# Performance work log

Hardware: AMD Instinct MI355X
Metric: run time of the kernel (lower is better)

The kernel has to match this reference:

```python
import jax, jax.numpy as jnp
import numpy as np

N_HEAD = 16

def rel_shift(x):
    # x: (qlen, klen, B, n). Pad one zero column at front of klen axis,
    # reinterpret as (klen+1, qlen, B, n), drop first row, reshape back.
    qlen, klen, b, n = x.shape
    x_pad = jnp.pad(x, ((0, 0), (1, 0), (0, 0), (0, 0)))
    x_pad = x_pad.reshape(klen + 1, qlen, b, n)
    return x_pad[1:].reshape(qlen, klen, b, n)

def setup_inputs() -> dict:
    key = jax.random.key(0)
    ks = jax.random.split(key, 9)
    qlen = klen = 1024
    B = 4
    d_model = 1024
    d_head = d_model // N_HEAD
    q = jax.random.normal(ks[0], (qlen, B, d_model), jnp.float32)
    K = jax.random.normal(ks[1], (klen, B, d_model), jnp.float32)
    V = jax.random.normal(ks[2], (klen, B, d_model), jnp.float32)
    mask = jax.random.bernoulli(ks[3], 0.1, (1, klen, B, 1))
    r = jax.random.normal(ks[4], (klen, d_model), jnp.float32)
    u = jax.random.normal(ks[5], (N_HEAD, d_head), jnp.float32) * 0.02
    v = jax.random.normal(ks[6], (N_HEAD, d_head), jnp.float32) * 0.02
    Wr = jax.random.normal(ks[7], (d_model, d_model), jnp.float32) / np.sqrt(d_model)
    br = jax.random.normal(ks[8], (d_model,), jnp.float32) * 0.02
    return {"q": q, "K": K, "V": V, "mask": mask, "r": r, "u": u, "v": v, "Wr": Wr, "br": br}

def reference(q, K, V, mask, r, u, v, Wr, br):
    qlen, bsz, d_model = q.shape
    klen = K.shape[0]
    d_head = d_model // N_HEAD
    qh = q.reshape(qlen, bsz, N_HEAD, d_head)
    Kh = K.reshape(klen, bsz, N_HEAD, d_head)
    Vh = V.reshape(klen, bsz, N_HEAD, d_head)
    rh = (r @ Wr.T + br).reshape(klen, N_HEAD, d_head)  # r_net projection
    AC = jnp.einsum('ibnd,jbnd->ijbn', qh + u, Kh)
    BD = rel_shift(jnp.einsum('ibnd,jnd->ijbn', qh + v, rh))
    score = (AC + BD) / jnp.sqrt(jnp.asarray(d_head, q.dtype))
    # mask (1,klen,B,1) broadcasts over qlen and heads (torch repeats over heads)
    score = jnp.where(mask, jnp.asarray(-1e9, score.dtype), score)
    weight = jax.nn.softmax(score, axis=1)
    out = jnp.einsum('ijbn,jbnd->ibnd', weight, Vh).reshape(qlen, bsz, d_model)
    return out, weight.mean(axis=-1)
```

## Files before the change

### kernel.cpp

```cpp
#include <hip/hip_runtime.h>
#include <hip/hip_fp16.h>
#include <stdint.h>


#define L 1024
#define BATCH 4
#define NH 16
#define DH 64
#define DM 1024
#define TI 16
#define NJT 16
#define BD_ST 1028
#define BDP_ST 1032
#define WT_ST 40
#define SCALE 0.125f
#define CS 0.18033688011112042f

typedef __attribute__((ext_vector_type(8))) short short8;
typedef __attribute__((ext_vector_type(4))) float f32x4;

static __device__ __forceinline__ unsigned short f2bf(float f) {
    union { float f; unsigned int u; } x; x.f = f;
    return (unsigned short)((x.u + 0x7fffu + ((x.u >> 16) & 1u)) >> 16);
}
static __device__ __forceinline__ float bf2f(unsigned short h) {
    union { unsigned int u; float f; } x; x.u = ((unsigned int)h) << 16;
    return x.f;
}
static __device__ __forceinline__ unsigned short f2h(float f) {
    __half h = __float2half(f);
    union { __half h; unsigned short s; } x; x.h = h; return x.s;
}
static __device__ __forceinline__ float h2f(unsigned short s) {
    union { __half h; unsigned short s; } x; x.s = s; return __half2float(x.h);
}
static __device__ __forceinline__ unsigned short* usp(void* base, int byteoff) {
    return (unsigned short*)((char*)base + byteoff);
}
static __device__ __forceinline__ short8 ld8(const void* base, int byteoff) {
    return *(const short8*)((const char*)base + byteoff);
}
static __device__ __forceinline__ float fexp2(float x) {
#if __has_builtin(__builtin_amdgcn_exp2f)
    return __builtin_amdgcn_exp2f(x);
#else
    return __expf(x * 0.6931471805599453f);
#endif
}
#define SW128(row, colByte) ((((row) * 128) + (colByte)) ^ (((row) & 7) << 4))

__global__ __launch_bounds__(256) void rh_gemm_mfma(
    const float* __restrict__ r, const float* __restrict__ Wr,
    const float* __restrict__ br, unsigned short* __restrict__ rhb)
{
    __shared__ unsigned short rT[64 * 64];
    __shared__ unsigned short wT[64 * 64];
    const int c0 = blockIdx.x * 64, m0 = blockIdx.y * 64;
    const int tid = threadIdx.x;
    const int w = tid >> 6, lane = tid & 63, lr = lane & 15, lg = lane >> 4;
    f32x4 acc[4] = {};

    for (int kt = 0; kt < 16; ++kt) {
        const int k0 = kt * 64;
        __syncthreads();
        const int row = tid >> 2, cb = (tid & 3) * 16;
#pragma unroll
        for (int q4 = 0; q4 < 4; ++q4) {
            float4 rv = *(const float4*)(r + (size_t)(c0 + row) * DM + k0 + cb + q4 * 4);
            unsigned short* p = usp(rT, SW128(row, (cb + q4 * 4) * 2));
            p[0] = f2bf(rv.x); p[1] = f2bf(rv.y); p[2] = f2bf(rv.z); p[3] = f2bf(rv.w);
            float4 wv = *(const float4*)(Wr + (size_t)(m0 + row) * DM + k0 + cb + q4 * 4);
            unsigned short* pw = usp(wT, SW128(row, (cb + q4 * 4) * 2));
            pw[0] = f2bf(wv.x); pw[1] = f2bf(wv.y); pw[2] = f2bf(wv.z); pw[3] = f2bf(wv.w);
        }
        __syncthreads();
#pragma unroll
        for (int mch = 0; mch < 4; ++mch)
#pragma unroll
            for (int kh = 0; kh < 2; ++kh) {
                short8 a  = ld8(rT, SW128(w * 16 + lr,   (kh * 32 + lg * 8) * 2));
                short8 bb = ld8(wT, SW128(mch * 16 + lr, (kh * 32 + lg * 8) * 2));
                acc[mch] = __builtin_amdgcn_mfma_f32_16x16x32_bf16(a, bb, acc[mch], 0, 0, 0);
            }
    }
#pragma unroll
    for (int mch = 0; mch < 4; ++mch)
#pragma unroll
        for (int r2 = 0; r2 < 4; ++r2) {
            const int c = c0 + w * 16 + lg * 4 + r2;
            const int d = mch * 16 + lr;
            const float val = acc[mch][r2] + br[m0 + d];
            rhb[((size_t)blockIdx.y * L + c) * DH + d] = f2bf(val);
        }
}

__global__ __launch_bounds__(256) void rh_gemm_kernel(
    const float* __restrict__ r, const float* __restrict__ Wr,
    const float* __restrict__ br, float* __restrict__ rhf)
{
    __shared__ float As[16][65];
    __shared__ float Bs[16][65];
    const int j0 = blockIdx.x * 64;
    const int m0 = blockIdx.y * 64;
    const int tid = threadIdx.x;
    const int ty = tid >> 4, tx = tid & 15;
    float acc[4][4] = {};

    for (int k0 = 0; k0 < DM; k0 += 16) {
        const int row = tid >> 2, c4 = (tid & 3) << 2;
        float4 av = *(const float4*)(r  + (size_t)(j0 + row) * DM + k0 + c4);
        float4 bv = *(const float4*)(Wr + (size_t)(m0 + row) * DM + k0 + c4);
        __syncthreads();
        As[c4 + 0][row] = av.x; As[c4 + 1][row] = av.y;
        As[c4 + 2][row] = av.z; As[c4 + 3][row] = av.w;
        Bs[c4 + 0][row] = bv.x; Bs[c4 + 1][row] = bv.y;
        Bs[c4 + 2][row] = bv.z; Bs[c4 + 3][row] = bv.w;
        __syncthreads();
#pragma unroll
        for (int k = 0; k < 16; ++k) {
            float a[4], bb[4];
#pragma unroll
            for (int t = 0; t < 4; ++t) { a[t] = As[k][ty * 4 + t]; bb[t] = Bs[k][tx * 4 + t]; }
#pragma unroll
            for (int ii = 0; ii < 4; ++ii)
#pragma unroll
                for (int jj = 0; jj < 4; ++jj)
                    acc[ii][jj] = fmaf(a[ii], bb[jj], acc[ii][jj]);
        }
    }
#pragma unroll
    for (int ii = 0; ii < 4; ++ii) {
        const int row = j0 + ty * 4 + ii;
#pragma unroll
        for (int jj = 0; jj < 4; ++jj) {
            const int col = m0 + tx * 4 + jj;
            rhf[(size_t)row * DM + col] = acc[ii][jj] + br[col];
        }
    }
}

__global__ __launch_bounds__(256) void prepass_kernel(
    const float* __restrict__ Kg, const float* __restrict__ Vg,
    unsigned short* __restrict__ Kbf, unsigned short* __restrict__ Vtb)
{
    __shared__ unsigned short tile[64][80];
    const int j0 = blockIdx.x * 64;
    const int b = blockIdx.y, n = blockIdx.z;
    const int bn = b * NH + n;
    const int tid = threadIdx.x;

    for (int idx = tid; idx < 64 * 16; idx += 256) {
        const int jr = idx >> 4, s4 = (idx & 15) * 4;
        const size_t src = ((size_t)(j0 + jr) * BATCH + b) * DM + n * DH + s4;
        float4 kv = *(const float4*)(Kg + src);
        ushort4 o;
        o.x = f2bf(kv.x); o.y = f2bf(kv.y); o.z = f2bf(kv.z); o.w = f2bf(kv.w);
        *(ushort4*)(Kbf + ((size_t)bn * L + j0 + jr) * DH + s4) = o;
        float4 vv4 = *(const float4*)(Vg + src);
        tile[s4 + 0][jr] = f2bf(vv4.x); tile[s4 + 1][jr] = f2bf(vv4.y);
        tile[s4 + 2][jr] = f2bf(vv4.z); tile[s4 + 3][jr] = f2bf(vv4.w);
    }
    __syncthreads();
    for (int idx = tid; idx < 64 * 8; idx += 256) {
        const int d = idx >> 3, p8 = (idx & 7) * 8;
        short8 o = *(const short8*)&tile[d][p8];
        *(short8*)(Vtb + ((size_t)bn * DH + d) * L + j0 + p8) = o;
    }
}

__global__ __launch_bounds__(256) void wm_reduce_kernel(
    const unsigned short* __restrict__ Wf, const float* __restrict__ rdeng,
    float* __restrict__ wm_out)
{
    const int ib = blockIdx.x;
    const int gq = blockIdx.y;
    const int b  = blockIdx.z;
    const int tid = threadIdx.x;
    const int w = tid >> 6, lane = tid & 63, lr = lane & 15, lg = lane >> 4;
    const int i = ib * 16 + lr;

    float rd[NH];
#pragma unroll
    for (int n = 0; n < NH; ++n)
        rd[n] = rdeng[((size_t)(b * NH + n) << 10) + i];

#pragma unroll
    for (int k = 0; k < 4; ++k) {
        const int gc = gq * 16 + w * 4 + k;
        float a0 = 0.f, a1 = 0.f, a2 = 0.f, a3 = 0.f;
#pragma unroll
        for (int n = 0; n < NH; ++n) {
            const int bn = b * NH + n;
            ushort4 wv = *(const ushort4*)(Wf +
                (((size_t)(bn * 64 + ib) * 64 + gc) * 64 + lane) * 4);
            a0 += bf2f(wv.x) * rd[n]; a1 += bf2f(wv.y) * rd[n];
            a2 += bf2f(wv.z) * rd[n]; a3 += bf2f(wv.w) * rd[n];
        }
        const size_t o = ((size_t)i * L + gc * 16 + lg * 4) * BATCH + b;
        wm_out[o]             = a0;
        wm_out[o + BATCH]     = a1;
        wm_out[o + 2 * BATCH] = a2;
        wm_out[o + 3 * BATCH] = a3;
    }
}

#define CHUNK_BODY(CHUNK, JC, KF0, KF1)                                       \
    {                                                                         \
        const int chunk_ = (CHUNK);                                           \
        const int jc_ = (JC);                                                 \
        short8 nk0_, nk1_;                                                    \
        const bool pf_ = (chunk_ + 2) < 16;                                   \
        if (pf_) {                                                            \
            const int jn_ = jwbase + (chunk_ + 2) * 16 + lr;                  \
            nk0_ = *(const short8*)(Kpane + (size_t)jn_ * DH + lg * 8);       \
            nk1_ = *(const short8*)(Kpane + (size_t)jn_ * DH + 32 + lg * 8);  \
        }                                                                     \
        f32x4 acc_ = {0.f, 0.f, 0.f, 0.f};                                    \
        acc_ = __builtin_amdgcn_mfma_f32_16x16x32_bf16(KF0, qu_a[0], acc_, 0, 0, 0); \
        acc_ = __builtin_amdgcn_mfma_f32_16x16x32_bf16(KF1, qu_a[1], acc_, 0, 0, 0); \
        const int jq_ = jc_ + lg * 4;                                         \
        const unsigned int m4_ = *(const unsigned int*)&mblk[jq_];            \
        const ushort4 bdq_ = *(const ushort4*)&BD[lr * BD_ST + jq_];          \
        ushort4 wpack_;                                                       \
        _Pragma("unroll")                                                     \
        for (int r2 = 0; r2 < 4; ++r2) {                                      \
            const unsigned short bdh_ =                                       \
                (r2 == 0) ? bdq_.x : (r2 == 1) ? bdq_.y : (r2 == 2) ? bdq_.z : bdq_.w; \
            const float mo_ = ((m4_ >> (8 * r2)) & 0xffu) ? -1e9f : 0.f;      \
            const float s_ = fminf(acc_[r2] + h2f(bdh_) + mo_, 126.f);        \
            const float wg_ = fexp2(s_);                                      \
            dl += wg_;                                                        \
            ((unsigned short*)&wpack_)[r2] = f2bf(wg_);                       \
        }                                                                     \
        *(ushort4*)(WtW + lr * WT_ST + ((jc_ >> 4) & 1) * 16 + lg * 4) = wpack_; \
        {          \
            union { ushort4 u4; unsigned long long u64; } cw_;                \
            cw_.u4 = wpack_;                                                  \
            __builtin_nontemporal_store(cw_.u64,                              \
                (unsigned long long*)(W_ws + wsbase + (((size_t)(jc_ >> 4)) * 64 + lane) * 4)); \
        }                                                                     \
        if (pf_) { KF0 = nk0_; KF1 = nk1_; }                                  \
    }

#define BD_BODY(CT, RB0, RB1)                                                 \
    {                                                                         \
        const int ct_ = (CT);                                                 \
        const int c0_ = ct_ * 64;                                             \
        short8 nr0_, nr1_;                                                    \
        const bool pf_ = (ct_ + 2) < 16;                                      \
        if (pf_) {                                                            \
            nr0_ = *(const short8*)(rpane + (size_t)((ct_ + 2) * 64 + ccol) * DH + lg * 8); \
            nr1_ = *(const short8*)(rpane + (size_t)((ct_ + 2) * 64 + ccol) * DH + 32 + lg * 8); \
        }                                                                     \
        f32x4 acc_ = {0.f, 0.f, 0.f, 0.f};                                    \
        acc_ = __builtin_amdgcn_mfma_f32_16x16x32_bf16(qv_a[0], RB0, acc_, 0, 0, 0); \
        acc_ = __builtin_amdgcn_mfma_f32_16x16x32_bf16(qv_a[1], RB1, acc_, 0, 0, 0); \
        const int c_ = c0_ + ccol;                                            \
        _Pragma("unroll")                                                     \
        for (int r2 = 0; r2 < 4; ++r2) {                                      \
            const int ilp_ = lg * 4 + r2;                                     \
            const unsigned short hv_ = f2h(acc_[r2]);                         \
            const int j1_ = c_ + i0 + ilp_ - 1023;                            \
            if (j1_ >= 0) BD[ilp_ * BD_ST + j1_] = hv_;                       \
            const int j2_ = c_ + i0 + ilp_ + 1;                               \
            if (ilp_ >= 1 && j2_ <= 1023) BD[(ilp_ - 1) * BD_ST + j2_] = hv_; \
        }                                                                     \
        {                           \
            short8 ra0_ = *(const short8*)(rpane + (size_t)(c0_ + col16) * DH + kq); \
            short8 ra1_ = *(const short8*)(rpane + (size_t)(c0_ + col16) * DH + kq + 8); \
            float s16_ = 0.f;                                                 \
            _Pragma("unroll")                                                 \
            for (int e = 0; e < 8; ++e) {                                     \
                s16_ = fmaf(qv16[e],     bf2f((unsigned short)ra0_[e]), s16_);\
                s16_ = fmaf(qv16[e + 8], bf2f((unsigned short)ra1_[e]), s16_);\
            }                                                                 \
            s16_ += __shfl_xor(s16_, 1);                                      \
            s16_ += __shfl_xor(s16_, 2);                                      \
            const int j16_ = c0_ + col16 + i0 + 17;                           \
            if ((tid & 3) == 0 && j16_ <= 1023)                               \
                BD[15 * BD_ST + j16_] = f2h(s16_);                            \
        }                                                                     \
        if (pf_) { RB0 = nr0_; RB1 = nr1_; }                                  \
    }

__global__ __launch_bounds__(256, 4) void attn_fused(
    const float* __restrict__ q,
    const unsigned short* __restrict__ Kbf, const unsigned short* __restrict__ Vtb,
    const unsigned char* __restrict__ maskp,
    const float* __restrict__ uu, const float* __restrict__ vvp,
    const unsigned short* __restrict__ rhb,
    float* __restrict__ out, unsigned short* __restrict__ W_ws,
    float* __restrict__ rdeng)
{
    __shared__ __align__(16) unsigned short BD[16 * BD_ST];
    __shared__ __align__(16) unsigned short Wt[4][16 * WT_ST];
    __shared__ unsigned char mblk[L];
    __shared__ float denomP[4][16];
    __shared__ float rdenom[16];
    __shared__ int mflags;

    const int lin = blockIdx.x;
    const int xcd = lin & 7, idx = lin >> 3;
    const int ib  = idx & 63;
    const int pane = xcd * 8 + (idx >> 6);
    const int b = pane >> 4, n = pane & 15;
    const int i0 = ib * 16;
    const int bn = pane;

    const int tid = threadIdx.x;
    const int w = tid >> 6, lane = tid & 63, lr = lane & 15, lg = lane >> 4;

    if (tid == 0) mflags = 0;
    __syncthreads();
    {
        int local = 0;
#pragma unroll 1
        for (int ww = tid; ww < 1024; ww += 256) {
            const unsigned int word = ((const unsigned int*)maskp)[ww];
            if (word == 0x3f800000u) local |= 1;
            else if (word & 0xffffff00u) local |= 2;
        }
        if (local) atomicOr(&mflags, local);
    }
    __syncthreads();
    {
        const int mtype = (mflags & 1) ? 2 : ((mflags & 2) ? 1 : 0);
#pragma unroll 1
        for (int j = tid; j < L; j += 256) {
            bool mv;
            if (mtype == 2)      mv = ((const float*)maskp)[j * BATCH + b] != 0.f;
            else if (mtype == 1) mv = maskp[j * BATCH + b] != 0;
            else                 mv = ((const int*)maskp)[j * BATCH + b] != 0;
            mblk[j] = mv ? 1 : 0;
        }
    }
    if (tid < 16) {
        const int jz = i0 + tid + 1;
        if (jz <= 1023) BD[tid * BD_ST + jz] = 0;
    }

    const float* qrow = q + ((size_t)(i0 + lr) * BATCH + b) * DM + n * DH;
    const float* urow = uu + n * DH;
    const float* vrow = vvp + n * DH;
    short8 qu_a[2], qv_a[2];
#pragma unroll
    for (int kh = 0; kh < 2; ++kh) {
        const int kb = kh * 32 + lg * 8;
        float4 qa = *(const float4*)(qrow + kb), qb = *(const float4*)(qrow + kb + 4);
        float4 ua = *(const float4*)(urow + kb), ub = *(const float4*)(urow + kb + 4);
        float4 va = *(const float4*)(vrow + kb), vb = *(const float4*)(vrow + kb + 4);
        short8 su, sv;
        su[0] = (short)f2bf((qa.x + ua.x) * CS); su[1] = (short)f2bf((qa.y + ua.y) * CS);
        su[2] = (short)f2bf((qa.z + ua.z) * CS); su[3] = (short)f2bf((qa.w + ua.w) * CS);
        su[4] = (short)f2bf((qb.x + ub.x) * CS); su[5] = (short)f2bf((qb.y + ub.y) * CS);
        su[6] = (short)f2bf((qb.z + ub.z) * CS); su[7] = (short)f2bf((qb.w + ub.w) * CS);
        sv[0] = (short)f2bf((qa.x + va.x) * CS); sv[1] = (short)f2bf((qa.y + va.y) * CS);
        sv[2] = (short)f2bf((qa.z + va.z) * CS); sv[3] = (short)f2bf((qa.w + va.w) * CS);
        sv[4] = (short)f2bf((qb.x + vb.x) * CS); sv[5] = (short)f2bf((qb.y + vb.y) * CS);
        sv[6] = (short)f2bf((qb.z + vb.z) * CS); sv[7] = (short)f2bf((qb.w + vb.w) * CS);
        qu_a[kh] = su; qv_a[kh] = sv;
    }
    float qv16[16];
    {
        const int kq0 = (tid & 3) * 16;
        if (i0 + 16 < L) {
            const float* q16 = q + ((size_t)(i0 + 16) * BATCH + b) * DM + n * DH;
#pragma unroll
            for (int e4 = 0; e4 < 4; ++e4) {
                float4 qa = *(const float4*)(q16 + kq0 + e4 * 4);
                float4 va = *(const float4*)(vrow + kq0 + e4 * 4);
                qv16[e4 * 4 + 0] = (qa.x + va.x) * CS; qv16[e4 * 4 + 1] = (qa.y + va.y) * CS;
                qv16[e4 * 4 + 2] = (qa.z + va.z) * CS; qv16[e4 * 4 + 3] = (qa.w + va.w) * CS;
            }
        } else {
#pragma unroll
            for (int e = 0; e < 16; ++e) qv16[e] = 0.f;
        }
    }

    {
        const unsigned short* rpane = rhb + (size_t)n * L * DH;
        const int ccol = w * 16 + lr;
        const int col16 = tid >> 2;
        const int kq = (tid & 3) * 16;
        short8 rbA0, rbA1, rbB0, rbB1;
        rbA0 = *(const short8*)(rpane + (size_t)ccol * DH + lg * 8);
        rbA1 = *(const short8*)(rpane + (size_t)ccol * DH + 32 + lg * 8);
        rbB0 = *(const short8*)(rpane + (size_t)(64 + ccol) * DH + lg * 8);
        rbB1 = *(const short8*)(rpane + (size_t)(64 + ccol) * DH + 32 + lg * 8);
#pragma unroll 1
        for (int ct2 = 0; ct2 < 8; ++ct2) {
            BD_BODY(ct2 * 2,     rbA0, rbA1);
            BD_BODY(ct2 * 2 + 1, rbB0, rbB1);
        }
    }
    __syncthreads();

    const unsigned short* Kpane = Kbf + (size_t)bn * L * DH;
    const unsigned short* Vpane = Vtb + (size_t)bn * DH * L;
    const int jwbase = w * 256;
    unsigned short* WtW = &Wt[w][0];
    f32x4 pv[4] = {};
    float dl = 0.f;
    const size_t wsbase = (((size_t)bn * 64 + ib) * 64) * 64 * 4;

    short8 kfA0, kfA1, kfB0, kfB1;
    kfA0 = *(const short8*)(Kpane + (size_t)(jwbase + lr) * DH + lg * 8);
    kfA1 = *(const short8*)(Kpane + (size_t)(jwbase + lr) * DH + 32 + lg * 8);
    kfB0 = *(const short8*)(Kpane + (size_t)(jwbase + 16 + lr) * DH + lg * 8);
    kfB1 = *(const short8*)(Kpane + (size_t)(jwbase + 16 + lr) * DH + 32 + lg * 8);

#pragma unroll 1
    for (int wi = 0; wi < 8; ++wi) {
        const int jbase32 = jwbase + wi * 32;
        short8 vf0, vf1, vf2, vf3;
        vf0 = *(const short8*)(Vpane + (size_t)(0 * 16 + lr) * L + jbase32 + lg * 8);
        vf1 = *(const short8*)(Vpane + (size_t)(1 * 16 + lr) * L + jbase32 + lg * 8);
        vf2 = *(const short8*)(Vpane + (size_t)(2 * 16 + lr) * L + jbase32 + lg * 8);
        vf3 = *(const short8*)(Vpane + (size_t)(3 * 16 + lr) * L + jbase32 + lg * 8);
        CHUNK_BODY(wi * 2,     jbase32,      kfA0, kfA1);
        CHUNK_BODY(wi * 2 + 1, jbase32 + 16, kfB0, kfB1);
        short8 afrag = *(const short8*)(WtW + lr * WT_ST + lg * 8);
        pv[0] = __builtin_amdgcn_mfma_f32_16x16x32_bf16(afrag, vf0, pv[0], 0, 0, 0);
        pv[1] = __builtin_amdgcn_mfma_f32_16x16x32_bf16(afrag, vf1, pv[1], 0, 0, 0);
        pv[2] = __builtin_amdgcn_mfma_f32_16x16x32_bf16(afrag, vf2, pv[2], 0, 0, 0);
        pv[3] = __builtin_amdgcn_mfma_f32_16x16x32_bf16(afrag, vf3, pv[3], 0, 0, 0);
    }

    dl += __shfl_xor(dl, 16, 64);
    dl += __shfl_xor(dl, 32, 64);
    if (lane < 16) denomP[w][lane] = dl;
    __syncthreads();

    {
        float* pvw = (float*)BD + w * 1024;
#pragma unroll
        for (int dch = 0; dch < 4; ++dch)
#pragma unroll
            for (int r2 = 0; r2 < 4; ++r2)
                pvw[(lg * 4 + r2) * 64 + dch * 16 + lr] = pv[dch][r2];
    }
    if (tid < 16) {
        const float dn = denomP[0][tid] + denomP[1][tid] + denomP[2][tid] + denomP[3][tid];
        rdenom[tid] = 1.f / dn;
        rdeng[((size_t)bn << 10) + i0 + tid] = 1.f / (dn * 16.f);
    }
    __syncthreads();

    {
        const float* pvwAll = (const float*)BD;
        const int il = tid >> 4, d0 = (tid & 15) * 4;
        float4 o  = *(const float4*)(pvwAll + 0 * 1024 + il * 64 + d0);
        float4 o1 = *(const float4*)(pvwAll + 1 * 1024 + il * 64 + d0);
        float4 o2 = *(const float4*)(pvwAll + 2 * 1024 + il * 64 + d0);
        float4 o3 = *(const float4*)(pvwAll + 3 * 1024 + il * 64 + d0);
        const float rs = rdenom[il];
        o.x = (o.x + o1.x + o2.x + o3.x) * rs;
        o.y = (o.y + o1.y + o2.y + o3.y) * rs;
        o.z = (o.z + o1.z + o2.z + o3.z) * rs;
        o.w = (o.w + o1.w + o2.w + o3.w) * rs;
        *(float4*)(out + ((size_t)(i0 + il) * BATCH + b) * DM + n * DH + d0) = o;
    }
}

template<int MODE>
__global__ __launch_bounds__(256, 2) void attn_legacy(
    const float* __restrict__ q,
    const void* __restrict__ Kp, const void* __restrict__ Vp,
    const unsigned char* __restrict__ maskp,
    const float* __restrict__ uu, const float* __restrict__ vvp,
    const void* __restrict__ rhp,
    float* __restrict__ out, float* __restrict__ wm_out)
{
    __shared__ unsigned short QU[16 * 64];
    __shared__ unsigned short QV[17 * 64];
    __shared__ unsigned short KR[(MODE == 1) ? 64 * 64 : 8];
    __shared__ unsigned short VT[(MODE == 1) ? 64 * 64 : 8];
    __shared__ unsigned short BDp[17 * BDP_ST];
    __shared__ unsigned short Wt[2][16 * 64];
    __shared__ unsigned char mblk[L];
    __shared__ float denomP[4][16];
    __shared__ float rdenom[16];
    __shared__ int mflags;

    const int i0 = blockIdx.x * TI;
    const int b  = blockIdx.y;
    const int n  = blockIdx.z;
    const int bn = b * NH + n;
    const int tid = threadIdx.x;
    const int w = tid >> 6, lane = tid & 63, lr = lane & 15, lg = lane >> 4;

    const unsigned short* Kbf = (const unsigned short*)Kp;
    const unsigned short* Vtb = (const unsigned short*)Vp;
    const unsigned short* rhb = (const unsigned short*)rhp;
    const float* Kg  = (const float*)Kp;
    const float* Vg  = (const float*)Vp;
    const float* rhf = (const float*)rhp;

    if (tid == 0) mflags = 0;
    __syncthreads();
    {
        int local = 0;
        for (int ww = tid; ww < 1024; ww += 256) {
            const unsigned int word = ((const unsigned int*)maskp)[ww];
            if (word == 0x3f800000u) local |= 1;
            else if (word & 0xffffff00u) local |= 2;
        }
        if (local) atomicOr(&mflags, local);
    }
    __syncthreads();
    {
        const int mtype = (mflags & 1) ? 2 : ((mflags & 2) ? 1 : 0);
        for (int j = tid; j < L; j += 256) {
            bool mv;
            if (mtype == 2)      mv = ((const float*)maskp)[j * BATCH + b] != 0.f;
            else if (mtype == 1) mv = maskp[j * BATCH + b] != 0;
            else                 mv = ((const int*)maskp)[j * BATCH + b] != 0;
            mblk[j] = mv ? 1 : 0;
        }
    }
    for (int idx = tid; idx < 17 * 64; idx += 256) {
        const int row = idx >> 6, d = idx & 63;
        const int gi = i0 + row;
        const float qval = (gi < L) ? q[((size_t)gi * BATCH + b) * DM + n * DH + d] : 0.f;
        *usp(QV, SW128(row, d * 2)) = f2bf((qval + vvp[n * DH + d]) * SCALE);
        if (row < 16) *usp(QU, SW128(row, d * 2)) = f2bf((qval + uu[n * DH + d]) * SCALE);
    }
    __syncthreads();

    for (int ct = 0; ct < 16; ++ct) {
        const int c0 = ct * 64;
        const int ccol = w * 16 + lr;
        if constexpr (MODE == 1) {
            __syncthreads();
            for (int idx = tid; idx < 64 * 16; idx += 256) {
                const int cr = idx >> 4, d4 = (idx & 15) * 4;
                float4 rv = *(const float4*)(rhf + (size_t)(c0 + cr) * DM + n * DH + d4);
                unsigned short* p = usp(KR, SW128(cr, d4 * 2));
                p[0] = f2bf(rv.x); p[1] = f2bf(rv.y); p[2] = f2bf(rv.z); p[3] = f2bf(rv.w);
            }
            __syncthreads();
        }
        f32x4 acc = {0.f, 0.f, 0.f, 0.f};
#pragma unroll
        for (int kh = 0; kh < 2; ++kh) {
            short8 a = ld8(QV, SW128(lr, (kh * 32 + lg * 8) * 2));
            short8 bb;
            if constexpr (MODE == 0)
                bb = *(const short8*)(rhb + ((size_t)n * L + c0 + ccol) * DH + kh * 32 + lg * 8);
            else
                bb = ld8(KR, SW128(ccol, (kh * 32 + lg * 8) * 2));
            acc = __builtin_amdgcn_mfma_f32_16x16x32_bf16(a, bb, acc, 0, 0, 0);
        }
#pragma unroll
        for (int r2 = 0; r2 < 4; ++r2)
            BDp[(lg * 4 + r2) * BDP_ST + c0 + ccol] = f2h(acc[r2]);
        {
            const int col = tid >> 2, kq = (tid & 3) * 16;
            float s16 = 0.f;
#pragma unroll
            for (int kk = 0; kk < 16; kk += 8) {
                short8 qa = ld8(QV, SW128(16, (kq + kk) * 2));
                short8 ra;
                if constexpr (MODE == 0)
                    ra = *(const short8*)(rhb + ((size_t)n * L + c0 + col) * DH + kq + kk);
                else
                    ra = ld8(KR, SW128(col, (kq + kk) * 2));
#pragma unroll
                for (int e = 0; e < 8; ++e)
                    s16 = fmaf(bf2f((unsigned short)qa[e]), bf2f((unsigned short)ra[e]), s16);
            }
            s16 += __shfl_xor(s16, 1);
            s16 += __shfl_xor(s16, 2);
            if ((tid & 3) == 0) BDp[16 * BDP_ST + c0 + col] = f2h(s16);
        }
    }

    const int jloc = w * 16 + lr;
    __syncthreads();

    f32x4 pv = {0.f, 0.f, 0.f, 0.f};
    float dl[4] = {0.f, 0.f, 0.f, 0.f};
    float tmp[4][NJT];
#pragma unroll
    for (int jt = 0; jt < NJT; ++jt) {
        const int j0 = jt * 64;
        const int gj = j0 + jloc;
        const int cur = jt & 1;
        if constexpr (MODE == 1) {
            __syncthreads();
            for (int idx = tid; idx < 64 * 16; idx += 256) {
                const int jr = idx >> 4, d4 = (idx & 15) * 4;
                const size_t src = ((size_t)(j0 + jr) * BATCH + b) * DM + n * DH + d4;
                float4 kv = *(const float4*)(Kg + src);
                unsigned short* p = usp(KR, SW128(jr, d4 * 2));
                p[0] = f2bf(kv.x); p[1] = f2bf(kv.y); p[2] = f2bf(kv.z); p[3] = f2bf(kv.w);
                float4 vv4 = *(const float4*)(Vg + src);
                *usp(VT, SW128(d4 + 0, jr * 2)) = f2bf(vv4.x);
                *usp(VT, SW128(d4 + 1, jr * 2)) = f2bf(vv4.y);
                *usp(VT, SW128(d4 + 2, jr * 2)) = f2bf(vv4.z);
                *usp(VT, SW128(d4 + 3, jr * 2)) = f2bf(vv4.w);
            }
            __syncthreads();
        }
        f32x4 acc = {0.f, 0.f, 0.f, 0.f};
#pragma unroll
        for (int kh = 0; kh < 2; ++kh) {
            short8 a = ld8(QU, SW128(lr, (kh * 32 + lg * 8) * 2));
            short8 bb;
            if constexpr (MODE == 0)
                bb = *(const short8*)(Kbf + ((size_t)bn * L + gj) * DH + kh * 32 + lg * 8);
            else
                bb = ld8(KR, SW128(jloc, (kh * 32 + lg * 8) * 2));
            acc = __builtin_amdgcn_mfma_f32_16x16x32_bf16(a, bb, acc, 0, 0, 0);
        }
        const bool msk = mblk[gj] != 0;
#pragma unroll
        for (int r2 = 0; r2 < 4; ++r2) {
            const int il = lg * 4 + r2;
            const int gi = i0 + il;
            const int t = gj - gi;
            float bd = 0.f;
            if (t != 1) {
                const int c = (t <= 0) ? (L - 1 + t) : (t - 2);
                bd = h2f(BDp[(il + (t >= 1 ? 1 : 0)) * BDP_ST + c]);
            }
            float s = acc[r2] + bd;
            if (msk) s = -1e9f;
            const float wgt = __expf(fminf(s, 80.f));
            dl[r2] += wgt;
            tmp[r2][jt] = wgt;
            *usp(Wt[cur], SW128(il, jloc * 2)) = f2bf(wgt);
        }
        __syncthreads();
#pragma unroll
        for (int kh = 0; kh < 2; ++kh) {
            short8 a = ld8(Wt[cur], SW128(lr, (kh * 32 + lg * 8) * 2));
            short8 bb;
            if constexpr (MODE == 0)
                bb = *(const short8*)(Vtb + ((size_t)bn * DH + jloc) * L + j0 + kh * 32 + lg * 8);
            else
                bb = ld8(VT, SW128(jloc, (kh * 32 + lg * 8) * 2));
            pv = __builtin_amdgcn_mfma_f32_16x16x32_bf16(a, bb, pv, 0, 0, 0);
        }
    }

#pragma unroll
    for (int r2 = 0; r2 < 4; ++r2) {
        float d = dl[r2];
        d += __shfl_xor(d, 1); d += __shfl_xor(d, 2);
        d += __shfl_xor(d, 4); d += __shfl_xor(d, 8);
        if (lr == 0) denomP[w][lg * 4 + r2] = d;
    }
    __syncthreads();
    if (tid < 16)
        rdenom[tid] = 1.f / (denomP[0][tid] + denomP[1][tid] + denomP[2][tid] + denomP[3][tid]);
    __syncthreads();

#pragma unroll
    for (int r2 = 0; r2 < 4; ++r2) {
        const int il = lg * 4 + r2;
        out[((size_t)(i0 + il) * BATCH + b) * DM + n * DH + w * 16 + lr] = pv[r2] * rdenom[il];
    }
#pragma unroll
    for (int r2 = 0; r2 < 4; ++r2) {
        const int il = lg * 4 + r2;
        const float rs = rdenom[il] * (1.f / 16.f);
#pragma unroll
        for (int jt = 0; jt < NJT; ++jt)
            atomicAdd(wm_out + ((size_t)(i0 + il) * L + jt * 64 + jloc) * BATCH + b,
                      tmp[r2][jt] * rs);
    }
}

extern "C" void kernel_launch(void* const* d_in, const int* in_sizes, int n_in,
                              void* d_out, int out_size, void* d_ws, size_t ws_size,
                              hipStream_t stream)
{
    (void)in_sizes; (void)n_in; (void)out_size;
    const float* q   = (const float*)d_in[0];
    const float* K   = (const float*)d_in[1];
    const float* V   = (const float*)d_in[2];
    const unsigned char* mask = (const unsigned char*)d_in[3];
    const float* r   = (const float*)d_in[4];
    const float* u   = (const float*)d_in[5];
    const float* v   = (const float*)d_in[6];
    const float* Wr  = (const float*)d_in[7];
    const float* br  = (const float*)d_in[8];

    float* out = (float*)d_out;
    float* wm  = out + (size_t)L * BATCH * DM;

    const size_t kvbytes = (size_t)BATCH * NH * L * DH * 2;
    const size_t rhbytes = (size_t)NH * L * DH * 2;
    const size_t wmbytes = (size_t)BATCH * NH * L * L * 2;
    const size_t rdbytes = (size_t)BATCH * NH * L * 4;

    if (ws_size >= 2 * kvbytes + rhbytes + wmbytes + rdbytes) {
        unsigned short* Kbf = (unsigned short*)d_ws;
        unsigned short* Vtb = Kbf + kvbytes / 2;
        unsigned short* rhb = Vtb + kvbytes / 2;
        unsigned short* Wws = rhb + rhbytes / 2;
        float* rdeng = (float*)(Wws + wmbytes / 2);
        rh_gemm_mfma<<<dim3(16, 16), 256, 0, stream>>>(r, Wr, br, rhb);
        prepass_kernel<<<dim3(16, 4, 16), 256, 0, stream>>>(K, V, Kbf, Vtb);
        attn_fused<<<dim3(4096), 256, 0, stream>>>(
            q, Kbf, Vtb, mask, u, v, rhb, out, Wws, rdeng);
        wm_reduce_kernel<<<dim3(64, 4, 4), 256, 0, stream>>>(Wws, rdeng, wm);
    } else if (ws_size >= 2 * kvbytes + rhbytes) {
        hipMemsetAsync(wm, 0, (size_t)L * L * BATCH * sizeof(float), stream);
        unsigned short* Kbf = (unsigned short*)d_ws;
        unsigned short* Vtb = Kbf + kvbytes / 2;
        unsigned short* rhb = Vtb + kvbytes / 2;
        rh_gemm_mfma<<<dim3(16, 16), 256, 0, stream>>>(r, Wr, br, rhb);
        prepass_kernel<<<dim3(16, 4, 16), 256, 0, stream>>>(K, V, Kbf, Vtb);
        attn_legacy<0><<<dim3(64, 4, 16), 256, 0, stream>>>(
            q, Kbf, Vtb, mask, u, v, rhb, out, wm);
    } else {
        hipMemsetAsync(wm, 0, (size_t)L * L * BATCH * sizeof(float), stream);
        float* rhf = (float*)d_ws;
        rh_gemm_kernel<<<dim3(16, 16), 256, 0, stream>>>(r, Wr, br, rhf);
        attn_legacy<1><<<dim3(64, 4, 16), 256, 0, stream>>>(
            q, K, V, mask, u, v, rhf, out, wm);
    }
}
```

Measured before the change: 293.7 us.

## Double attn_fused block to 512 threads and prebake mask into BD tile

Widens the fused attention block from 4 to 8 wavefronts, so each wave handles half as many key columns in both the BD projection and the softmax/PV loops, and the final cross-wave reduction sums 8 partials. The per-element mask select is removed from the hot loop: masked key columns are written as half-precision negative infinity into the BD shared tile before the score pass. The legacy fallback kernels and workspace-size checks are deleted, so the fused path always runs. The larger block raises per-block register and shared-memory demand and adds an extra barrier, and the fallback for small workspaces is gone.

```diff
diff --git a/kernel.cpp b/kernel.cpp
--- a/kernel.cpp
+++ b/kernel.cpp
@@ -15,6 +15,7 @@
 #define WT_ST 40
 #define SCALE 0.125f
 #define CS 0.18033688011112042f
+#define HNEGINF 0xFC00u
 
 typedef __attribute__((ext_vector_type(8))) short short8;
 typedef __attribute__((ext_vector_type(4))) float f32x4;
@@ -94,51 +95,6 @@
         }
 }
 
-__global__ __launch_bounds__(256) void rh_gemm_kernel(
-    const float* __restrict__ r, const float* __restrict__ Wr,
-    const float* __restrict__ br, float* __restrict__ rhf)
-{
-    __shared__ float As[16][65];
-    __shared__ float Bs[16][65];
-    const int j0 = blockIdx.x * 64;
-    const int m0 = blockIdx.y * 64;
-    const int tid = threadIdx.x;
-    const int ty = tid >> 4, tx = tid & 15;
-    float acc[4][4] = {};
-
-    for (int k0 = 0; k0 < DM; k0 += 16) {
-        const int row = tid >> 2, c4 = (tid & 3) << 2;
-        float4 av = *(const float4*)(r  + (size_t)(j0 + row) * DM + k0 + c4);
-        float4 bv = *(const float4*)(Wr + (size_t)(m0 + row) * DM + k0 + c4);
-        __syncthreads();
-        As[c4 + 0][row] = av.x; As[c4 + 1][row] = av.y;
-        As[c4 + 2][row] = av.z; As[c4 + 3][row] = av.w;
-        Bs[c4 + 0][row] = bv.x; Bs[c4 + 1][row] = bv.y;
-        Bs[c4 + 2][row] = bv.z; Bs[c4 + 3][row] = bv.w;
-        __syncthreads();
-#pragma unroll
-        for (int k = 0; k < 16; ++k) {
-            float a[4], bb[4];
-#pragma unroll
-            for (int t = 0; t < 4; ++t) { a[t] = As[k][ty * 4 + t]; bb[t] = Bs[k][tx * 4 + t]; }
-#pragma unroll
-            for (int ii = 0; ii < 4; ++ii)
-#pragma unroll
-                for (int jj = 0; jj < 4; ++jj)
-                    acc[ii][jj] = fmaf(a[ii], bb[jj], acc[ii][jj]);
-        }
-    }
-#pragma unroll
-    for (int ii = 0; ii < 4; ++ii) {
-        const int row = j0 + ty * 4 + ii;
-#pragma unroll
-        for (int jj = 0; jj < 4; ++jj) {
-            const int col = m0 + tx * 4 + jj;
-            rhf[(size_t)row * DM + col] = acc[ii][jj] + br[col];
-        }
-    }
-}
-
 __global__ __launch_bounds__(256) void prepass_kernel(
     const float* __restrict__ Kg, const float* __restrict__ Vg,
     unsigned short* __restrict__ Kbf, unsigned short* __restrict__ Vtb)
@@ -209,7 +165,7 @@
         const int chunk_ = (CHUNK);                                           \
         const int jc_ = (JC);                                                 \
         short8 nk0_, nk1_;                                                    \
-        const bool pf_ = (chunk_ + 2) < 16;                                   \
+        const bool pf_ = (chunk_ + 2) < 8;                                    \
         if (pf_) {                                                            \
             const int jn_ = jwbase + (chunk_ + 2) * 16 + lr;                  \
             nk0_ = *(const short8*)(Kpane + (size_t)jn_ * DH + lg * 8);       \
@@ -219,21 +175,19 @@
         acc_ = __builtin_amdgcn_mfma_f32_16x16x32_bf16(KF0, qu_a[0], acc_, 0, 0, 0); \
         acc_ = __builtin_amdgcn_mfma_f32_16x16x32_bf16(KF1, qu_a[1], acc_, 0, 0, 0); \
         const int jq_ = jc_ + lg * 4;                                         \
-        const unsigned int m4_ = *(const unsigned int*)&mblk[jq_];            \
         const ushort4 bdq_ = *(const ushort4*)&BD[lr * BD_ST + jq_];          \
         ushort4 wpack_;                                                       \
         _Pragma("unroll")                                                     \
         for (int r2 = 0; r2 < 4; ++r2) {                                      \
             const unsigned short bdh_ =                                       \
                 (r2 == 0) ? bdq_.x : (r2 == 1) ? bdq_.y : (r2 == 2) ? bdq_.z : bdq_.w; \
-            const float mo_ = ((m4_ >> (8 * r2)) & 0xffu) ? -1e9f : 0.f;      \
-            const float s_ = fminf(acc_[r2] + h2f(bdh_) + mo_, 126.f);        \
+            const float s_ = fminf(acc_[r2] + h2f(bdh_), 126.f);              \
             const float wg_ = fexp2(s_);                                      \
             dl += wg_;                                                        \
             ((unsigned short*)&wpack_)[r2] = f2bf(wg_);                       \
         }                                                                     \
         *(ushort4*)(WtW + lr * WT_ST + ((jc_ >> 4) & 1) * 16 + lg * 4) = wpack_; \
-        {          \
+        {                                         \
             union { ushort4 u4; unsigned long long u64; } cw_;                \
             cw_.u4 = wpack_;                                                  \
             __builtin_nontemporal_store(cw_.u64,                              \
@@ -245,12 +199,12 @@
 #define BD_BODY(CT, RB0, RB1)                                                 \
     {                                                                         \
         const int ct_ = (CT);                                                 \
-        const int c0_ = ct_ * 64;                                             \
+        const int c0_ = ct_ * 128;                                            \
         short8 nr0_, nr1_;                                                    \
-        const bool pf_ = (ct_ + 2) < 16;                                      \
+        const bool pf_ = (ct_ + 2) < 8;                                       \
         if (pf_) {                                                            \
-            nr0_ = *(const short8*)(rpane + (size_t)((ct_ + 2) * 64 + ccol) * DH + lg * 8); \
-            nr1_ = *(const short8*)(rpane + (size_t)((ct_ + 2) * 64 + ccol) * DH + 32 + lg * 8); \
+            nr0_ = *(const short8*)(rpane + (size_t)((ct_ + 2) * 128 + ccol) * DH + lg * 8); \
+            nr1_ = *(const short8*)(rpane + (size_t)((ct_ + 2) * 128 + ccol) * DH + 32 + lg * 8); \
         }                                                                     \
         f32x4 acc_ = {0.f, 0.f, 0.f, 0.f};                                    \
         acc_ = __builtin_amdgcn_mfma_f32_16x16x32_bf16(qv_a[0], RB0, acc_, 0, 0, 0); \
@@ -265,7 +219,7 @@
             const int j2_ = c_ + i0 + ilp_ + 1;                               \
             if (ilp_ >= 1 && j2_ <= 1023) BD[(ilp_ - 1) * BD_ST + j2_] = hv_; \
         }                                                                     \
-        {                           \
+        {         \
             short8 ra0_ = *(const short8*)(rpane + (size_t)(c0_ + col16) * DH + kq); \
             short8 ra1_ = *(const short8*)(rpane + (size_t)(c0_ + col16) * DH + kq + 8); \
             float s16_ = 0.f;                                                 \
@@ -283,7 +237,7 @@
         if (pf_) { RB0 = nr0_; RB1 = nr1_; }                                  \
     }
 
-__global__ __launch_bounds__(256, 4) void attn_fused(
+__global__ __launch_bounds__(512, 6) void attn_fused(
     const float* __restrict__ q,
     const unsigned short* __restrict__ Kbf, const unsigned short* __restrict__ Vtb,
     const unsigned char* __restrict__ maskp,
@@ -293,9 +247,9 @@
     float* __restrict__ rdeng)
 {
     __shared__ __align__(16) unsigned short BD[16 * BD_ST];
-    __shared__ __align__(16) unsigned short Wt[4][16 * WT_ST];
+    __shared__ __align__(16) unsigned short Wt[8][16 * WT_ST];
     __shared__ unsigned char mblk[L];
-    __shared__ float denomP[4][16];
+    __shared__ float denomP[8][16];
     __shared__ float rdenom[16];
     __shared__ int mflags;
 
@@ -315,7 +269,7 @@
     {
         int local = 0;
 #pragma unroll 1
-        for (int ww = tid; ww < 1024; ww += 256) {
+        for (int ww = tid; ww < 1024; ww += 512) {
             const unsigned int word = ((const unsigned int*)maskp)[ww];
             if (word == 0x3f800000u) local |= 1;
             else if (word & 0xffffff00u) local |= 2;
@@ -326,7 +280,7 @@
     {
         const int mtype = (mflags & 1) ? 2 : ((mflags & 2) ? 1 : 0);
 #pragma unroll 1
-        for (int j = tid; j < L; j += 256) {
+        for (int j = tid; j < L; j += 512) {
             bool mv;
             if (mtype == 2)      mv = ((const float*)maskp)[j * BATCH + b] != 0.f;
             else if (mtype == 1) mv = maskp[j * BATCH + b] != 0;
@@ -386,19 +340,29 @@
         short8 rbA0, rbA1, rbB0, rbB1;
         rbA0 = *(const short8*)(rpane + (size_t)ccol * DH + lg * 8);
         rbA1 = *(const short8*)(rpane + (size_t)ccol * DH + 32 + lg * 8);
-        rbB0 = *(const short8*)(rpane + (size_t)(64 + ccol) * DH + lg * 8);
-        rbB1 = *(const short8*)(rpane + (size_t)(64 + ccol) * DH + 32 + lg * 8);
+        rbB0 = *(const short8*)(rpane + (size_t)(128 + ccol) * DH + lg * 8);
+        rbB1 = *(const short8*)(rpane + (size_t)(128 + ccol) * DH + 32 + lg * 8);
 #pragma unroll 1
-        for (int ct2 = 0; ct2 < 8; ++ct2) {
+        for (int ct2 = 0; ct2 < 4; ++ct2) {
             BD_BODY(ct2 * 2,     rbA0, rbA1);
             BD_BODY(ct2 * 2 + 1, rbB0, rbB1);
         }
     }
     __syncthreads();
 
+#pragma unroll 1
+    for (int j = tid; j < L; j += 512) {
+        if (mblk[j]) {
+#pragma unroll
+            for (int il = 0; il < 16; ++il)
+                BD[il * BD_ST + j] = (unsigned short)HNEGINF;
+        }
+    }
+    __syncthreads();
+
     const unsigned short* Kpane = Kbf + (size_t)bn * L * DH;
     const unsigned short* Vpane = Vtb + (size_t)bn * DH * L;
-    const int jwbase = w * 256;
+    const int jwbase = w * 128;
     unsigned short* WtW = &Wt[w][0];
     f32x4 pv[4] = {};
     float dl = 0.f;
@@ -411,7 +375,7 @@
     kfB1 = *(const short8*)(Kpane + (size_t)(jwbase + 16 + lr) * DH + 32 + lg * 8);
 
 #pragma unroll 1
-    for (int wi = 0; wi < 8; ++wi) {
+    for (int wi = 0; wi < 4; ++wi) {
         const int jbase32 = jwbase + wi * 32;
         short8 vf0, vf1, vf2, vf3;
         vf0 = *(const short8*)(Vpane + (size_t)(0 * 16 + lr) * L + jbase32 + lg * 8);
@@ -441,235 +405,25 @@
                 pvw[(lg * 4 + r2) * 64 + dch * 16 + lr] = pv[dch][r2];
     }
     if (tid < 16) {
-        const float dn = denomP[0][tid] + denomP[1][tid] + denomP[2][tid] + denomP[3][tid];
+        const float dn = denomP[0][tid] + denomP[1][tid] + denomP[2][tid] + denomP[3][tid]
+                       + denomP[4][tid] + denomP[5][tid] + denomP[6][tid] + denomP[7][tid];
         rdenom[tid] = 1.f / dn;
         rdeng[((size_t)bn << 10) + i0 + tid] = 1.f / (dn * 16.f);
     }
     __syncthreads();
 
-    {
+    if (tid < 256) {
         const float* pvwAll = (const float*)BD;
         const int il = tid >> 4, d0 = (tid & 15) * 4;
-        float4 o  = *(const float4*)(pvwAll + 0 * 1024 + il * 64 + d0);
-        float4 o1 = *(const float4*)(pvwAll + 1 * 1024 + il * 64 + d0);
-        float4 o2 = *(const float4*)(pvwAll + 2 * 1024 + il * 64 + d0);
-        float4 o3 = *(const float4*)(pvwAll + 3 * 1024 + il * 64 + d0);
+        float4 o = *(const float4*)(pvwAll + il * 64 + d0);
+#pragma unroll
+        for (int ww = 1; ww < 8; ++ww) {
+            float4 ox = *(const float4*)(pvwAll + ww * 1024 + il * 64 + d0);
+            o.x += ox.x; o.y += ox.y; o.z += ox.z; o.w += ox.w;
+        }
         const float rs = rdenom[il];
-        o.x = (o.x + o1.x + o2.x + o3.x) * rs;
-        o.y = (o.y + o1.y + o2.y + o3.y) * rs;
-        o.z = (o.z + o1.z + o2.z + o3.z) * rs;
-        o.w = (o.w + o1.w + o2.w + o3.w) * rs;
+        o.x *= rs; o.y *= rs; o.z *= rs; o.w *= rs;
         *(float4*)(out + ((size_t)(i0 + il) * BATCH + b) * DM + n * DH + d0) = o;
-    }
-}
-
-template<int MODE>
-__global__ __launch_bounds__(256, 2) void attn_legacy(
-    const float* __restrict__ q,
-    const void* __restrict__ Kp, const void* __restrict__ Vp,
-    const unsigned char* __restrict__ maskp,
-    const float* __restrict__ uu, const float* __restrict__ vvp,
-    const void* __restrict__ rhp,
-    float* __restrict__ out, float* __restrict__ wm_out)
-{
-    __shared__ unsigned short QU[16 * 64];
-    __shared__ unsigned short QV[17 * 64];
-    __shared__ unsigned short KR[(MODE == 1) ? 64 * 64 : 8];
-    __shared__ unsigned short VT[(MODE == 1) ? 64 * 64 : 8];
-    __shared__ unsigned short BDp[17 * BDP_ST];
-    __shared__ unsigned short Wt[2][16 * 64];
-    __shared__ unsigned char mblk[L];
-    __shared__ float denomP[4][16];
-    __shared__ float rdenom[16];
-    __shared__ int mflags;
-
-    const int i0 = blockIdx.x * TI;
-    const int b  = blockIdx.y;
-    const int n  = blockIdx.z;
-    const int bn = b * NH + n;
-    const int tid = threadIdx.x;
-    const int w = tid >> 6, lane = tid & 63, lr = lane & 15, lg = lane >> 4;
-
-    const unsigned short* Kbf = (const unsigned short*)Kp;
-    const unsigned short* Vtb = (const unsigned short*)Vp;
-    const unsigned short* rhb = (const unsigned short*)rhp;
-    const float* Kg  = (const float*)Kp;
-    const float* Vg  = (const float*)Vp;
-    const float* rhf = (const float*)rhp;
-
-    if (tid == 0) mflags = 0;
-    __syncthreads();
-    {
-        int local = 0;
-        for (int ww = tid; ww < 1024; ww += 256) {
-            const unsigned int word = ((const unsigned int*)maskp)[ww];
-            if (word == 0x3f800000u) local |= 1;
-            else if (word & 0xffffff00u) local |= 2;
-        }
-        if (local) atomicOr(&mflags, local);
-    }
-    __syncthreads();
-    {
-        const int mtype = (mflags & 1) ? 2 : ((mflags & 2) ? 1 : 0);
-        for (int j = tid; j < L; j += 256) {
-            bool mv;
-            if (mtype == 2)      mv = ((const float*)maskp)[j * BATCH + b] != 0.f;
-            else if (mtype == 1) mv = maskp[j * BATCH + b] != 0;
-            else                 mv = ((const int*)maskp)[j * BATCH + b] != 0;
-            mblk[j] = mv ? 1 : 0;
-        }
-    }
-    for (int idx = tid; idx < 17 * 64; idx += 256) {
-        const int row = idx >> 6, d = idx & 63;
-        const int gi = i0 + row;
-        const float qval = (gi < L) ? q[((size_t)gi * BATCH + b) * DM + n * DH + d] : 0.f;
-        *usp(QV, SW128(row, d * 2)) = f2bf((qval + vvp[n * DH + d]) * SCALE);
-        if (row < 16) *usp(QU, SW128(row, d * 2)) = f2bf((qval + uu[n * DH + d]) * SCALE);
-    }
-    __syncthreads();
-
-    for (int ct = 0; ct < 16; ++ct) {
-        const int c0 = ct * 64;
-        const int ccol = w * 16 + lr;
-        if constexpr (MODE == 1) {
-            __syncthreads();
-            for (int idx = tid; idx < 64 * 16; idx += 256) {
-                const int cr = idx >> 4, d4 = (idx & 15) * 4;
-                float4 rv = *(const float4*)(rhf + (size_t)(c0 + cr) * DM + n * DH + d4);
-                unsigned short* p = usp(KR, SW128(cr, d4 * 2));
-                p[0] = f2bf(rv.x); p[1] = f2bf(rv.y); p[2] = f2bf(rv.z); p[3] = f2bf(rv.w);
-            }
-            __syncthreads();
-        }
-        f32x4 acc = {0.f, 0.f, 0.f, 0.f};
-#pragma unroll
-        for (int kh = 0; kh < 2; ++kh) {
-            short8 a = ld8(QV, SW128(lr, (kh * 32 + lg * 8) * 2));
-            short8 bb;
-            if constexpr (MODE == 0)
-                bb = *(const short8*)(rhb + ((size_t)n * L + c0 + ccol) * DH + kh * 32 + lg * 8);
-            else
-                bb = ld8(KR, SW128(ccol, (kh * 32 + lg * 8) * 2));
-            acc = __builtin_amdgcn_mfma_f32_16x16x32_bf16(a, bb, acc, 0, 0, 0);
-        }
-#pragma unroll
-        for (int r2 = 0; r2 < 4; ++r2)
-            BDp[(lg * 4 + r2) * BDP_ST + c0 + ccol] = f2h(acc[r2]);
-        {
-            const int col = tid >> 2, kq = (tid & 3) * 16;
-            float s16 = 0.f;
-#pragma unroll
-            for (int kk = 0; kk < 16; kk += 8) {
-                short8 qa = ld8(QV, SW128(16, (kq + kk) * 2));
-                short8 ra;
-                if constexpr (MODE == 0)
-                    ra = *(const short8*)(rhb + ((size_t)n * L + c0 + col) * DH + kq + kk);
-                else
-                    ra = ld8(KR, SW128(col, (kq + kk) * 2));
-#pragma unroll
-                for (int e = 0; e < 8; ++e)
-                    s16 = fmaf(bf2f((unsigned short)qa[e]), bf2f((unsigned short)ra[e]), s16);
-            }
-            s16 += __shfl_xor(s16, 1);
-            s16 += __shfl_xor(s16, 2);
-            if ((tid & 3) == 0) BDp[16 * BDP_ST + c0 + col] = f2h(s16);
-        }
-    }
-
-    const int jloc = w * 16 + lr;
-    __syncthreads();
-
-    f32x4 pv = {0.f, 0.f, 0.f, 0.f};
-    float dl[4] = {0.f, 0.f, 0.f, 0.f};
-    float tmp[4][NJT];
-#pragma unroll
-    for (int jt = 0; jt < NJT; ++jt) {
-        const int j0 = jt * 64;
-        const int gj = j0 + jloc;
-        const int cur = jt & 1;
-        if constexpr (MODE == 1) {
-            __syncthreads();
-            for (int idx = tid; idx < 64 * 16; idx += 256) {
-                const int jr = idx >> 4, d4 = (idx & 15) * 4;
-                const size_t src = ((size_t)(j0 + jr) * BATCH + b) * DM + n * DH + d4;
-                float4 kv = *(const float4*)(Kg + src);
-                unsigned short* p = usp(KR, SW128(jr, d4 * 2));
-                p[0] = f2bf(kv.x); p[1] = f2bf(kv.y); p[2] = f2bf(kv.z); p[3] = f2bf(kv.w);
-                float4 vv4 = *(const float4*)(Vg + src);
-                *usp(VT, SW128(d4 + 0, jr * 2)) = f2bf(vv4.x);
-                *usp(VT, SW128(d4 + 1, jr * 2)) = f2bf(vv4.y);
-                *usp(VT, SW128(d4 + 2, jr * 2)) = f2bf(vv4.z);
-                *usp(VT, SW128(d4 + 3, jr * 2)) = f2bf(vv4.w);
-            }
-            __syncthreads();
-        }
-        f32x4 acc = {0.f, 0.f, 0.f, 0.f};
-#pragma unroll
-        for (int kh = 0; kh < 2; ++kh) {
-            short8 a = ld8(QU, SW128(lr, (kh * 32 + lg * 8) * 2));
-            short8 bb;
-            if constexpr (MODE == 0)
-                bb = *(const short8*)(Kbf + ((size_t)bn * L + gj) * DH + kh * 32 + lg * 8);
-            else
-                bb = ld8(KR, SW128(jloc, (kh * 32 + lg * 8) * 2));
-            acc = __builtin_amdgcn_mfma_f32_16x16x32_bf16(a, bb, acc, 0, 0, 0);
-        }
-        const bool msk = mblk[gj] != 0;
-#pragma unroll
-        for (int r2 = 0; r2 < 4; ++r2) {
-            const int il = lg * 4 + r2;
-            const int gi = i0 + il;
-            const int t = gj - gi;
-            float bd = 0.f;
-            if (t != 1) {
-                const int c = (t <= 0) ? (L - 1 + t) : (t - 2);
-                bd = h2f(BDp[(il + (t >= 1 ? 1 : 0)) * BDP_ST + c]);
-            }
-            float s = acc[r2] + bd;
-            if (msk) s = -1e9f;
-            const float wgt = __expf(fminf(s, 80.f));
-            dl[r2] += wgt;
-            tmp[r2][jt] = wgt;
-            *usp(Wt[cur], SW128(il, jloc * 2)) = f2bf(wgt);
-        }
-        __syncthreads();
-#pragma unroll
-        for (int kh = 0; kh < 2; ++kh) {
-            short8 a = ld8(Wt[cur], SW128(lr, (kh * 32 + lg * 8) * 2));
-            short8 bb;
-            if constexpr (MODE == 0)
-                bb = *(const short8*)(Vtb + ((size_t)bn * DH + jloc) * L + j0 + kh * 32 + lg * 8);
-            else
-                bb = ld8(VT, SW128(jloc, (kh * 32 + lg * 8) * 2));
-            pv = __builtin_amdgcn_mfma_f32_16x16x32_bf16(a, bb, pv, 0, 0, 0);
-        }
-    }
-
-#pragma unroll
-    for (int r2 = 0; r2 < 4; ++r2) {
-        float d = dl[r2];
-        d += __shfl_xor(d, 1); d += __shfl_xor(d, 2);
-        d += __shfl_xor(d, 4); d += __shfl_xor(d, 8);
-        if (lr == 0) denomP[w][lg * 4 + r2] = d;
-    }
-    __syncthreads();
-    if (tid < 16)
-        rdenom[tid] = 1.f / (denomP[0][tid] + denomP[1][tid] + denomP[2][tid] + denomP[3][tid]);
-    __syncthreads();
-
-#pragma unroll
-    for (int r2 = 0; r2 < 4; ++r2) {
-        const int il = lg * 4 + r2;
-        out[((size_t)(i0 + il) * BATCH + b) * DM + n * DH + w * 16 + lr] = pv[r2] * rdenom[il];
-    }
-#pragma unroll
-    for (int r2 = 0; r2 < 4; ++r2) {
-        const int il = lg * 4 + r2;
-        const float rs = rdenom[il] * (1.f / 16.f);
-#pragma unroll
-        for (int jt = 0; jt < NJT; ++jt)
-            atomicAdd(wm_out + ((size_t)(i0 + il) * L + jt * 64 + jloc) * BATCH + b,
-                      tmp[r2][jt] * rs);
     }
 }
 
@@ -677,7 +431,7 @@
                               void* d_out, int out_size, void* d_ws, size_t ws_size,
                               hipStream_t stream)
 {
-    (void)in_sizes; (void)n_in; (void)out_size;
+    (void)in_sizes; (void)n_in; (void)out_size; (void)ws_size;
     const float* q   = (const float*)d_in[0];
     const float* K   = (const float*)d_in[1];
     const float* V   = (const float*)d_in[2];
@@ -694,33 +448,16 @@
     const size_t kvbytes = (size_t)BATCH * NH * L * DH * 2;
     const size_t rhbytes = (size_t)NH * L * DH * 2;
     const size_t wmbytes = (size_t)BATCH * NH * L * L * 2;
-    const size_t rdbytes = (size_t)BATCH * NH * L * 4;
-
-    if (ws_size >= 2 * kvbytes + rhbytes + wmbytes + rdbytes) {
-        unsigned short* Kbf = (unsigned short*)d_ws;
-        unsigned short* Vtb = Kbf + kvbytes / 2;
-        unsigned short* rhb = Vtb + kvbytes / 2;
-        unsigned short* Wws = rhb + rhbytes / 2;
-        float* rdeng = (float*)(Wws + wmbytes / 2);
-        rh_gemm_mfma<<<dim3(16, 16), 256, 0, stream>>>(r, Wr, br, rhb);
-        prepass_kernel<<<dim3(16, 4, 16), 256, 0, stream>>>(K, V, Kbf, Vtb);
-        attn_fused<<<dim3(4096), 256, 0, stream>>>(
-            q, Kbf, Vtb, mask, u, v, rhb, out, Wws, rdeng);
-        wm_reduce_kernel<<<dim3(64, 4, 4), 256, 0, stream>>>(Wws, rdeng, wm);
-    } else if (ws_size >= 2 * kvbytes + rhbytes) {
-        hipMemsetAsync(wm, 0, (size_t)L * L * BATCH * sizeof(float), stream);
-        unsigned short* Kbf = (unsigned short*)d_ws;
-        unsigned short* Vtb = Kbf + kvbytes / 2;
-        unsigned short* rhb = Vtb + kvbytes / 2;
-        rh_gemm_mfma<<<dim3(16, 16), 256, 0, stream>>>(r, Wr, br, rhb);
-        prepass_kernel<<<dim3(16, 4, 16), 256, 0, stream>>>(K, V, Kbf, Vtb);
-        attn_legacy<0><<<dim3(64, 4, 16), 256, 0, stream>>>(
-            q, Kbf, Vtb, mask, u, v, rhb, out, wm);
-    } else {
-        hipMemsetAsync(wm, 0, (size_t)L * L * BATCH * sizeof(float), stream);
-        float* rhf = (float*)d_ws;
-        rh_gemm_kernel<<<dim3(16, 16), 256, 0, stream>>>(r, Wr, br, rhf);
-        attn_legacy<1><<<dim3(64, 4, 16), 256, 0, stream>>>(
-            q, K, V, mask, u, v, rhf, out, wm);
-    }
-}
+
+    unsigned short* Kbf = (unsigned short*)d_ws;
+    unsigned short* Vtb = Kbf + kvbytes / 2;
+    unsigned short* rhb = Vtb + kvbytes / 2;
+    unsigned short* Wws = rhb + rhbytes / 2;
+    float* rdeng = (float*)(Wws + wmbytes / 2);
+
+    rh_gemm_mfma<<<dim3(16, 16), 256, 0, stream>>>(r, Wr, br, rhb);
+    prepass_kernel<<<dim3(16, 4, 16), 256, 0, stream>>>(K, V, Kbf, Vtb);
+    attn_fused<<<dim3(4096), 512, 0, stream>>>(
+        q, Kbf, Vtb, mask, u, v, rhb, out, Wws, rdeng);
+    wm_reduce_kernel<<<dim3(64, 4, 4), 256, 0, stream>>>(Wws, rdeng, wm);
+}
```

New measurement: 442.6 us. +50.7%, slower.
